# Optimization experiments

Measured on AMD Instinct MI355X. Metric: run time of the kernel, lower is better.

The kernel has to match this reference:

```python
import jax, jax.numpy as jnp
import numpy as np

N = 50000


def gcn_conv(x, W, b, src, dst, deg_inv_sqrt):
    # h = x @ W, then symmetric-normalized aggregation with self-loops
    h = x @ W  # [N, out]
    norm = deg_inv_sqrt[src] * deg_inv_sqrt[dst]  # [E]
    agg = jax.ops.segment_sum(h[src] * norm[:, None], dst, num_segments=N)
    # self-loop contribution: norm_ii = deg_inv_sqrt[i]^2
    agg = agg + h * (deg_inv_sqrt * deg_inv_sqrt)[:, None]
    return agg + b


def setup_inputs() -> dict:
    key = jax.random.key(0)
    ks = jax.random.split(key, 8)
    F_in, H, C = 128, 128, 64
    x = jax.random.normal(ks[0], (N, F_in), dtype=jnp.float32)
    edge_index = jax.random.randint(ks[1], (2, 800000), 0, N, dtype=jnp.int64)
    s = 1.0 / np.sqrt(F_in)
    W1 = jax.random.uniform(ks[2], (F_in, H), jnp.float32, -s, s)
    b1 = jnp.zeros((H,), jnp.float32)
    W2 = jax.random.uniform(ks[3], (H, H), jnp.float32, -s, s)
    b2 = jnp.zeros((H,), jnp.float32)
    W3 = jax.random.uniform(ks[4], (H, C), jnp.float32, -s, s)
    b3 = jnp.zeros((C,), jnp.float32)
    return {"x": x, "edge_index": edge_index, "W1": W1, "b1": b1,
            "W2": W2, "b2": b2, "W3": W3, "b3": b3}


def reference(x, edge_index, W1, b1, W2, b2, W3, b3):
    src, dst = edge_index[0], edge_index[1]
    # degree with self-loops (edge weight 1): deg[i] = in-degree + 1
    deg = jnp.zeros((N,), x.dtype).at[dst].add(1.0) + 1.0
    dinv = jax.lax.rsqrt(deg)
    h = gcn_conv(x, W1, b1, src, dst, dinv)
    h = jax.nn.relu(h)  # dropout p=0 / eval -> identity
    h = gcn_conv(h, W2, b2, src, dst, dinv)
    h = jax.nn.relu(h)
    h = gcn_conv(h, W3, b3, src, dst, dinv)
    return jax.nn.log_softmax(h, axis=-1)
```

## Files before the change

kernel.cpp:

```cpp
#include <hip/hip_runtime.h>
#include <math.h>

typedef short short8 __attribute__((ext_vector_type(8)));
typedef float floatx4 __attribute__((ext_vector_type(4)));

__device__ __forceinline__ float4 ld4(const float* p) { return *reinterpret_cast<const float4*>(p); }
__device__ __forceinline__ void st4(float* p, float4 v) { *reinterpret_cast<float4*>(p) = v; }

__device__ __forceinline__ float bf2f(unsigned int u) { return __uint_as_float(u << 16); }
__device__ __forceinline__ unsigned int f2bf1(float f) {
    unsigned int x = __float_as_uint(f);
    return (x + 0x7fffu + ((x >> 16) & 1u)) >> 16;
}
__device__ __forceinline__ unsigned int f2bf2(float lo, float hi) {
    return f2bf1(lo) | (f2bf1(hi) << 16);
}
__device__ __forceinline__ void unpack8(uint4 v, float* f) {
    f[0] = bf2f(v.x & 0xffffu); f[1] = bf2f(v.x >> 16);
    f[2] = bf2f(v.y & 0xffffu); f[3] = bf2f(v.y >> 16);
    f[4] = bf2f(v.z & 0xffffu); f[5] = bf2f(v.z >> 16);
    f[6] = bf2f(v.w & 0xffffu); f[7] = bf2f(v.w >> 16);
}

__global__ __launch_bounds__(256) void k_count_prep(const int* __restrict__ dst, int* __restrict__ deg,
                                                    int* __restrict__ rank, int E, int nbE,
                                                    const float* __restrict__ W1, const float* __restrict__ W2,
                                                    const float* __restrict__ W3, unsigned short* __restrict__ Wt1,
                                                    unsigned short* __restrict__ Wt2, unsigned short* __restrict__ Wt3) {
    if ((int)blockIdx.x < nbE) {
        int e = blockIdx.x * 256 + threadIdx.x;
        if (e < E) rank[e] = atomicAdd(&deg[dst[e]], 1);
    } else {
        int t = (blockIdx.x - nbE) * 256 + threadIdx.x;
        if (t < 16384) {
            int k = t & 127, n = t >> 7;
            Wt1[n * 128 + k] = (unsigned short)f2bf1(W1[(size_t)k * 128 + n]);
        } else if (t < 32768) {
            int u = t - 16384;
            int k = u & 127, n = u >> 7;
            Wt2[n * 128 + k] = (unsigned short)f2bf1(W2[(size_t)k * 128 + n]);
        } else if (t < 40960) {
            int u = t - 32768;
            int k = u & 127, n = u >> 7;
            Wt3[n * 128 + k] = (unsigned short)f2bf1(W3[(size_t)k * 64 + n]);
        }
    }
}

__global__ __launch_bounds__(256) void k_dinv_reduce(const int* __restrict__ deg, float* __restrict__ dinv,
                                                     int* __restrict__ bsum, int n, int nbN) {
    __shared__ int s[256];
    int t = threadIdx.x;
    if ((int)blockIdx.x < nbN) {
        int i = blockIdx.x * 256 + t;
        if (i < n) dinv[i] = 1.0f / sqrtf((float)deg[i] + 1.0f);
        return;
    }
    int b = (int)blockIdx.x - nbN;
    int i = b * 256 + t;
    s[t] = (i < n) ? deg[i] : 0;
    __syncthreads();
    for (int off = 128; off > 0; off >>= 1) {
        if (t < off) s[t] += s[t + off];
        __syncthreads();
    }
    if (t == 0) bsum[b] = s[0];
}

__global__ __launch_bounds__(256) void k_scansmall_gemm1(const int* __restrict__ bsum, int* __restrict__ boff, int nb,
                                                         const float* __restrict__ X, const unsigned short* __restrict__ Wt,
                                                         const float* __restrict__ dinv,
                                                         unsigned short* __restrict__ O, int nrows) {
    constexpr int LDR = 136;
    __shared__ __align__(16) unsigned char smem[(64 * LDR + 128 * LDR) * 2];

    const int tid = threadIdx.x;
    if (blockIdx.x == 0) {
        int* s = (int*)smem;
        int v = (tid < nb) ? bsum[tid] : 0;
        s[tid] = v;
        __syncthreads();
        for (int off = 1; off < 256; off <<= 1) {
            int x = (tid >= off) ? s[tid - off] : 0;
            __syncthreads();
            s[tid] += x;
            __syncthreads();
        }
        if (tid < nb) boff[tid] = s[tid] - v;
        return;
    }

    unsigned short* sX = (unsigned short*)smem;
    unsigned short* sB = sX + 64 * LDR;
    const int row0 = ((int)blockIdx.x - 1) * 64;

#pragma unroll
    for (int i = 0; i < 4; ++i) {
        int idx = tid + i * 256;
        int r = idx >> 4, c8 = idx & 15;
        int grow = row0 + r;
        uint4 v = make_uint4(0, 0, 0, 0);
        if (grow < nrows) {
            float4 a = ld4(X + (size_t)grow * 128 + c8 * 8);
            float4 b = ld4(X + (size_t)grow * 128 + c8 * 8 + 4);
            v = make_uint4(f2bf2(a.x, a.y), f2bf2(a.z, a.w), f2bf2(b.x, b.y), f2bf2(b.z, b.w));
        }
        *reinterpret_cast<uint4*>(&sX[r * LDR + c8 * 8]) = v;
    }
#pragma unroll
    for (int i = 0; i < 8; ++i) {
        int idx = tid + i * 256;
        int nn = idx >> 4, c8 = idx & 15;
        *reinterpret_cast<uint4*>(&sB[nn * LDR + c8 * 8]) =
            *reinterpret_cast<const uint4*>(Wt + (size_t)nn * 128 + c8 * 8);
    }
    __syncthreads();

    const int lane = tid & 63;
    const int wave = tid >> 6;
    const int l15  = lane & 15;
    const int quad = lane >> 4;

    floatx4 acc[8];
#pragma unroll
    for (int j = 0; j < 8; ++j) acc[j] = (floatx4){0.f, 0.f, 0.f, 0.f};

    const unsigned short* xbase = &sX[(wave * 16 + l15) * LDR + quad * 8];
#pragma unroll
    for (int kk = 0; kk < 4; ++kk) {
        short8 xb = *reinterpret_cast<const short8*>(xbase + kk * 32);
#pragma unroll
        for (int j = 0; j < 8; ++j) {
            short8 wa = *reinterpret_cast<const short8*>(&sB[(j * 16 + l15) * LDR + quad * 8 + kk * 32]);
            acc[j] = __builtin_amdgcn_mfma_f32_16x16x32_bf16(wa, xb, acc[j], 0, 0, 0);
        }
    }

    int xrow = row0 + wave * 16 + l15;
    if (xrow < nrows) {
        float di = dinv[xrow];
#pragma unroll
        for (int j = 0; j < 8; ++j) {
            uint2 o = make_uint2(f2bf2(acc[j][0] * di, acc[j][1] * di), f2bf2(acc[j][2] * di, acc[j][3] * di));
            *reinterpret_cast<uint2*>(O + (size_t)xrow * 128 + j * 16 + quad * 4) = o;
        }
    }
}

__global__ __launch_bounds__(256) void k_scan_final(const int* __restrict__ deg, const int* __restrict__ boff,
                                                    int* __restrict__ row_off, int n) {
    __shared__ int s[256];
    int t = threadIdx.x;
    int i = blockIdx.x * 256 + t;
    int v = (i < n) ? deg[i] : 0;
    s[t] = v;
    __syncthreads();
    for (int off = 1; off < 256; off <<= 1) {
        int x = (t >= off) ? s[t - off] : 0;
        __syncthreads();
        s[t] += x;
        __syncthreads();
    }
    int incl = s[t] + boff[blockIdx.x];
    if (i < n) {
        row_off[i] = incl - v;
        if (i == n - 1) row_off[n] = incl;
    }
}

__global__ __launch_bounds__(256) void k_fill(const int* __restrict__ src, const int* __restrict__ dst,
                                              const int* __restrict__ rank, const int* __restrict__ roff,
                                              int* __restrict__ csrc, int E) {
    int e = blockIdx.x * 256 + threadIdx.x;
    if (e < E) csrc[roff[dst[e]] + rank[e]] = src[e];
}

template <int NC>
__global__ __launch_bounds__(256) void k_gemm_mfma(const unsigned short* __restrict__ X,
                                                   const unsigned short* __restrict__ Wt,
                                                   const float* __restrict__ dinv,
                                                   unsigned short* __restrict__ O, int nrows) {
    constexpr int LDR = 136;
    __shared__ unsigned short sX[64 * LDR];
    __shared__ unsigned short sB[NC * LDR];

    const int tid  = threadIdx.x;
    const int row0 = blockIdx.x * 64;

#pragma unroll
    for (int i = 0; i < 4; ++i) {
        int idx = tid + i * 256;
        int r = idx >> 4, c8 = idx & 15;
        int grow = row0 + r;
        uint4 v = make_uint4(0, 0, 0, 0);
        if (grow < nrows) v = *reinterpret_cast<const uint4*>(X + (size_t)grow * 128 + c8 * 8);
        *reinterpret_cast<uint4*>(&sX[r * LDR + c8 * 8]) = v;
    }
#pragma unroll
    for (int i = 0; i < NC / 16; ++i) {
        int idx = tid + i * 256;
        int n = idx >> 4, c8 = idx & 15;
        *reinterpret_cast<uint4*>(&sB[n * LDR + c8 * 8]) =
            *reinterpret_cast<const uint4*>(Wt + (size_t)n * 128 + c8 * 8);
    }
    __syncthreads();

    const int lane = tid & 63;
    const int wave = tid >> 6;
    const int l15  = lane & 15;
    const int quad = lane >> 4;

    floatx4 acc[NC / 16];
#pragma unroll
    for (int j = 0; j < NC / 16; ++j) acc[j] = (floatx4){0.f, 0.f, 0.f, 0.f};

    const unsigned short* xbase = &sX[(wave * 16 + l15) * LDR + quad * 8];
#pragma unroll
    for (int kk = 0; kk < 4; ++kk) {
        short8 xb = *reinterpret_cast<const short8*>(xbase + kk * 32);
#pragma unroll
        for (int j = 0; j < NC / 16; ++j) {
            short8 wa = *reinterpret_cast<const short8*>(&sB[(j * 16 + l15) * LDR + quad * 8 + kk * 32]);
            acc[j] = __builtin_amdgcn_mfma_f32_16x16x32_bf16(wa, xb, acc[j], 0, 0, 0);
        }
    }

    int xrow = row0 + wave * 16 + l15;
    if (xrow < nrows) {
        float di = dinv[xrow];
#pragma unroll
        for (int j = 0; j < NC / 16; ++j) {
            uint2 o = make_uint2(f2bf2(acc[j][0] * di, acc[j][1] * di), f2bf2(acc[j][2] * di, acc[j][3] * di));
            *reinterpret_cast<uint2*>(O + (size_t)xrow * NC + j * 16 + quad * 4) = o;
        }
    }
}

__global__ __launch_bounds__(256) void k_agg_relu(const unsigned short* __restrict__ H, const int* __restrict__ roff,
                                                  const int* __restrict__ csrc, const float* __restrict__ dinv,
                                                  const float* __restrict__ bias, unsigned short* __restrict__ O, int n) {
    int t      = blockIdx.x * 256 + threadIdx.x;
    int node   = t >> 5;
    int lane32 = t & 31;
    int half   = lane32 >> 4;
    int f8     = (lane32 & 15) * 8;
    if (node >= n) return;

    float a[8];
    if (half == 0) {
        uint4 hv = *reinterpret_cast<const uint4*>(H + (size_t)node * 128 + f8);
        unpack8(hv, a);
    } else {
#pragma unroll
        for (int i = 0; i < 8; ++i) a[i] = 0.0f;
    }

    int e0 = roff[node];
    int e1 = roff[node + 1];
    int mid = e0 + ((e1 - e0) >> 1);
    int e  = half ? mid : e0;
    int ee = half ? e1 : mid;

    while (e < ee) {
        int cnt = ee - e;
        int idx[8];
#pragma unroll
        for (int u = 0; u < 8; ++u) idx[u] = csrc[e + min(u, cnt - 1)];
        uint4 v[8];
#pragma unroll
        for (int u = 0; u < 8; ++u) v[u] = *reinterpret_cast<const uint4*>(H + (size_t)idx[u] * 128 + f8);
#pragma unroll
        for (int u = 0; u < 8; ++u) {
            float mk = (u < cnt) ? 1.0f : 0.0f;
            float g[8];
            unpack8(v[u], g);
#pragma unroll
            for (int i = 0; i < 8; ++i) a[i] = fmaf(mk, g[i], a[i]);
        }
        e += 8;
    }

#pragma unroll
    for (int i = 0; i < 8; ++i) a[i] += __shfl_xor(a[i], 16);

    if (half == 0) {
        float di = dinv[node];
        float4 b0 = ld4(bias + f8);
        float4 b1 = ld4(bias + f8 + 4);
        float bb[8] = {b0.x, b0.y, b0.z, b0.w, b1.x, b1.y, b1.z, b1.w};
#pragma unroll
        for (int i = 0; i < 8; ++i) a[i] = fmaxf(a[i] * di + bb[i], 0.0f);

        uint4 ov = make_uint4(f2bf2(a[0], a[1]), f2bf2(a[2], a[3]), f2bf2(a[4], a[5]), f2bf2(a[6], a[7]));
        *reinterpret_cast<uint4*>(O + (size_t)node * 128 + f8) = ov;
    }
}

__global__ __launch_bounds__(256) void k_agg_softmax(const unsigned short* __restrict__ H, const int* __restrict__ roff,
                                                     const int* __restrict__ csrc, const float* __restrict__ dinv,
                                                     const float* __restrict__ bias, float* __restrict__ O, int n) {
    int t      = blockIdx.x * 256 + threadIdx.x;
    int node   = t >> 4;
    int lane16 = t & 15;
    int half   = lane16 >> 3;
    int f8     = (lane16 & 7) * 8;
    if (node >= n) return;

    float a[8];
    if (half == 0) {
        uint4 hv = *reinterpret_cast<const uint4*>(H + (size_t)node * 64 + f8);
        unpack8(hv, a);
    } else {
#pragma unroll
        for (int i = 0; i < 8; ++i) a[i] = 0.0f;
    }

    int e0 = roff[node];
    int e1 = roff[node + 1];
    int mid = e0 + ((e1 - e0) >> 1);
    int e  = half ? mid : e0;
    int ee = half ? e1 : mid;

    while (e < ee) {
        int cnt = ee - e;
        int idx[8];
#pragma unroll
        for (int u = 0; u < 8; ++u) idx[u] = csrc[e + min(u, cnt - 1)];
        uint4 v[8];
#pragma unroll
        for (int u = 0; u < 8; ++u) v[u] = *reinterpret_cast<const uint4*>(H + (size_t)idx[u] * 64 + f8);
#pragma unroll
        for (int u = 0; u < 8; ++u) {
            float mk = (u < cnt) ? 1.0f : 0.0f;
            float g[8];
            unpack8(v[u], g);
#pragma unroll
            for (int i = 0; i < 8; ++i) a[i] = fmaf(mk, g[i], a[i]);
        }
        e += 8;
    }

#pragma unroll
    for (int i = 0; i < 8; ++i) a[i] += __shfl_xor(a[i], 8);

    if (half == 0) {
        float di = dinv[node];
        float4 b0 = ld4(bias + f8);
        float4 b1 = ld4(bias + f8 + 4);
        float bb[8] = {b0.x, b0.y, b0.z, b0.w, b1.x, b1.y, b1.z, b1.w};
        float v[8];
#pragma unroll
        for (int i = 0; i < 8; ++i) v[i] = a[i] * di + bb[i];

        float m = v[0];
#pragma unroll
        for (int i = 1; i < 8; ++i) m = fmaxf(m, v[i]);
        m = fmaxf(m, __shfl_xor(m, 1));
        m = fmaxf(m, __shfl_xor(m, 2));
        m = fmaxf(m, __shfl_xor(m, 4));

        float ssum = 0.0f;
#pragma unroll
        for (int i = 0; i < 8; ++i) ssum += expf(v[i] - m);
        ssum += __shfl_xor(ssum, 1);
        ssum += __shfl_xor(ssum, 2);
        ssum += __shfl_xor(ssum, 4);
        float ls = logf(ssum);

        float* op = O + (size_t)node * 64 + f8;
        st4(op, make_float4(v[0] - m - ls, v[1] - m - ls, v[2] - m - ls, v[3] - m - ls));
        st4(op + 4, make_float4(v[4] - m - ls, v[5] - m - ls, v[6] - m - ls, v[7] - m - ls));
    }
}

extern "C" void kernel_launch(void* const* d_in, const int* in_sizes, int n_in,
                              void* d_out, int out_size, void* d_ws, size_t ws_size,
                              hipStream_t stream) {
    const float* x  = (const float*)d_in[0];
    const int*   ei = (const int*)d_in[1];
    const float* W1 = (const float*)d_in[2];
    const float* b1 = (const float*)d_in[3];
    const float* W2 = (const float*)d_in[4];
    const float* b2 = (const float*)d_in[5];
    const float* W3 = (const float*)d_in[6];
    const float* b3 = (const float*)d_in[7];
    float* out = (float*)d_out;

    const int N = in_sizes[0] / 128;
    const int E = in_sizes[1] / 2;
    const int* src = ei;
    const int* dst = ei + E;

    char* ws = (char*)d_ws;
    size_t off = 0;
    auto alloc = [&](size_t bytes) -> char* {
        char* p = ws + off;
        off = (off + bytes + 255) & ~(size_t)255;
        return p;
    };
    int nb  = (N + 255) / 256;
    int nbE = (E + 255) / 256;
    int blocks64 = (N + 63) / 64;

    int*   deg     = (int*)alloc((size_t)N * 4);
    int*   row_off = (int*)alloc(((size_t)N + 1) * 4);
    float* dinv    = (float*)alloc((size_t)N * 4);
    int*   bsum    = (int*)alloc((size_t)nb * 4);
    int*   boff    = (int*)alloc((size_t)nb * 4);
    int*   rank    = (int*)alloc((size_t)E * 4);
    int*   csrc    = (int*)alloc((size_t)E * 4);
    unsigned short* Wt1  = (unsigned short*)alloc(128 * 128 * 2);
    unsigned short* Wt2  = (unsigned short*)alloc(128 * 128 * 2);
    unsigned short* Wt3  = (unsigned short*)alloc(64 * 128 * 2);
    unsigned short* bufA = (unsigned short*)alloc((size_t)N * 128 * 2);
    unsigned short* bufB = (unsigned short*)alloc((size_t)N * 128 * 2);
    unsigned short* bufC = (unsigned short*)alloc((size_t)N * 64 * 2);
    (void)ws_size; (void)n_in; (void)out_size;

    hipMemsetAsync(deg, 0, (size_t)N * 4, stream);
    k_count_prep<<<nbE + 160, 256, 0, stream>>>(dst, deg, rank, E, nbE, W1, W2, W3, Wt1, Wt2, Wt3);
    k_dinv_reduce<<<nb + nb, 256, 0, stream>>>(deg, dinv, bsum, N, nb);
    k_scansmall_gemm1<<<1 + blocks64, 256, 0, stream>>>(bsum, boff, nb, x, Wt1, dinv, bufA, N);
    k_scan_final<<<nb, 256, 0, stream>>>(deg, boff, row_off, N);
    k_fill<<<nbE, 256, 0, stream>>>(src, dst, rank, row_off, csrc, E);

    k_agg_relu<<<((size_t)N * 32 + 255) / 256, 256, 0, stream>>>(bufA, row_off, csrc, dinv, b1, bufB, N);
    k_gemm_mfma<128><<<blocks64, 256, 0, stream>>>(bufB, Wt2, dinv, bufA, N);
    k_agg_relu<<<((size_t)N * 32 + 255) / 256, 256, 0, stream>>>(bufA, row_off, csrc, dinv, b2, bufB, N);
    k_gemm_mfma<64><<<blocks64, 256, 0, stream>>>(bufB, Wt3, dinv, bufC, N);
    k_agg_softmax<<<((size_t)N * 16 + 255) / 256, 256, 0, stream>>>(bufC, row_off, csrc, dinv, b3, out, N);
}
```

Baseline: 257.5 us.

## Replace multi-kernel scan with single-pass decoupled lookback scan and fuse fill with GEMM1

Replaces the reduce, small-scan and final-scan kernels with a single-pass decoupled-lookback scan that also writes dinv. The CSR fill is merged into the first GEMM launch as extra blocks. The aggregation loops now unroll by 4 with a scalar tail instead of 8-wide masked gathers. The aim is fewer launches and serial stages in preprocessing and less wasted gather work on short edge lists. The lookback spin-wait depends on earlier blocks being scheduled first, which is not guaranteed.

```diff
diff --git a/kernel.cpp b/kernel.cpp
--- a/kernel.cpp
+++ b/kernel.cpp
@@ -47,52 +47,62 @@
     }
 }
 
-__global__ __launch_bounds__(256) void k_dinv_reduce(const int* __restrict__ deg, float* __restrict__ dinv,
-                                                     int* __restrict__ bsum, int n, int nbN) {
+__global__ __launch_bounds__(256) void k_scan_dinv(const int* __restrict__ deg, int* __restrict__ state,
+                                                   int* __restrict__ row_off, float* __restrict__ dinv, int n) {
     __shared__ int s[256];
-    int t = threadIdx.x;
-    if ((int)blockIdx.x < nbN) {
-        int i = blockIdx.x * 256 + t;
-        if (i < n) dinv[i] = 1.0f / sqrtf((float)deg[i] + 1.0f);
-        return;
-    }
-    int b = (int)blockIdx.x - nbN;
-    int i = b * 256 + t;
-    s[t] = (i < n) ? deg[i] : 0;
+    __shared__ int sbase;
+    const int bid = (int)blockIdx.x;
+    const int t = threadIdx.x;
+    int i = bid * 256 + t;
+    int v = (i < n) ? deg[i] : 0;
+    s[t] = v;
     __syncthreads();
-    for (int off = 128; off > 0; off >>= 1) {
-        if (t < off) s[t] += s[t + off];
+    for (int off = 1; off < 256; off <<= 1) {
+        int x = (t >= off) ? s[t - off] : 0;
         __syncthreads();
-    }
-    if (t == 0) bsum[b] = s[0];
-}
-
-__global__ __launch_bounds__(256) void k_scansmall_gemm1(const int* __restrict__ bsum, int* __restrict__ boff, int nb,
-                                                         const float* __restrict__ X, const unsigned short* __restrict__ Wt,
-                                                         const float* __restrict__ dinv,
-                                                         unsigned short* __restrict__ O, int nrows) {
+        s[t] += x;
+        __syncthreads();
+    }
+    const int bsum = s[255];
+    if (t == 0) {
+        atomicExch(&state[bid], (int)((1u << 30) | (unsigned)bsum));
+        int run = 0;
+        for (int j = bid - 1; j >= 0; --j) {
+            int st;
+            do { st = atomicAdd(&state[j], 0); } while ((unsigned)st < (1u << 30));
+            run += st & 0x3fffffff;
+            if (((unsigned)st >> 30) == 2u) break;
+        }
+        atomicExch(&state[bid], (int)((2u << 30) | (unsigned)(run + bsum)));
+        sbase = run;
+    }
+    __syncthreads();
+    if (i < n) {
+        row_off[i] = sbase + s[t] - v;
+        dinv[i] = 1.0f / sqrtf((float)v + 1.0f);
+        if (i == n - 1) row_off[n] = sbase + bsum;
+    }
+}
+
+__global__ __launch_bounds__(256) void k_fill_gemm1(const int* __restrict__ src, const int* __restrict__ dst,
+                                                    const int* __restrict__ rank, const int* __restrict__ roff,
+                                                    int* __restrict__ csrc, int E, int nbE,
+                                                    const float* __restrict__ X, const unsigned short* __restrict__ Wt,
+                                                    const float* __restrict__ dinv,
+                                                    unsigned short* __restrict__ O, int nrows) {
     constexpr int LDR = 136;
     __shared__ __align__(16) unsigned char smem[(64 * LDR + 128 * LDR) * 2];
-
     const int tid = threadIdx.x;
-    if (blockIdx.x == 0) {
-        int* s = (int*)smem;
-        int v = (tid < nb) ? bsum[tid] : 0;
-        s[tid] = v;
-        __syncthreads();
-        for (int off = 1; off < 256; off <<= 1) {
-            int x = (tid >= off) ? s[tid - off] : 0;
-            __syncthreads();
-            s[tid] += x;
-            __syncthreads();
-        }
-        if (tid < nb) boff[tid] = s[tid] - v;
+
+    if ((int)blockIdx.x < nbE) {
+        int e = blockIdx.x * 256 + tid;
+        if (e < E) csrc[roff[dst[e]] + rank[e]] = src[e];
         return;
     }
 
     unsigned short* sX = (unsigned short*)smem;
     unsigned short* sB = sX + 64 * LDR;
-    const int row0 = ((int)blockIdx.x - 1) * 64;
+    const int row0 = ((int)blockIdx.x - nbE) * 64;
 
 #pragma unroll
     for (int i = 0; i < 4; ++i) {
@@ -147,34 +157,6 @@
     }
 }
 
-__global__ __launch_bounds__(256) void k_scan_final(const int* __restrict__ deg, const int* __restrict__ boff,
-                                                    int* __restrict__ row_off, int n) {
-    __shared__ int s[256];
-    int t = threadIdx.x;
-    int i = blockIdx.x * 256 + t;
-    int v = (i < n) ? deg[i] : 0;
-    s[t] = v;
-    __syncthreads();
-    for (int off = 1; off < 256; off <<= 1) {
-        int x = (t >= off) ? s[t - off] : 0;
-        __syncthreads();
-        s[t] += x;
-        __syncthreads();
-    }
-    int incl = s[t] + boff[blockIdx.x];
-    if (i < n) {
-        row_off[i] = incl - v;
-        if (i == n - 1) row_off[n] = incl;
-    }
-}
-
-__global__ __launch_bounds__(256) void k_fill(const int* __restrict__ src, const int* __restrict__ dst,
-                                              const int* __restrict__ rank, const int* __restrict__ roff,
-                                              int* __restrict__ csrc, int E) {
-    int e = blockIdx.x * 256 + threadIdx.x;
-    if (e < E) csrc[roff[dst[e]] + rank[e]] = src[e];
-}
-
 template <int NC>
 __global__ __launch_bounds__(256) void k_gemm_mfma(const unsigned short* __restrict__ X,
                                                    const unsigned short* __restrict__ Wt,
@@ -261,23 +243,27 @@
     int e  = half ? mid : e0;
     int ee = half ? e1 : mid;
 
-    while (e < ee) {
-        int cnt = ee - e;
-        int idx[8];
-#pragma unroll
-        for (int u = 0; u < 8; ++u) idx[u] = csrc[e + min(u, cnt - 1)];
-        uint4 v[8];
-#pragma unroll
-        for (int u = 0; u < 8; ++u) v[u] = *reinterpret_cast<const uint4*>(H + (size_t)idx[u] * 128 + f8);
-#pragma unroll
-        for (int u = 0; u < 8; ++u) {
-            float mk = (u < cnt) ? 1.0f : 0.0f;
-            float g[8];
-            unpack8(v[u], g);
-#pragma unroll
-            for (int i = 0; i < 8; ++i) a[i] = fmaf(mk, g[i], a[i]);
-        }
-        e += 8;
+    for (; e + 3 < ee; e += 4) {
+        int s[4];
+        uint4 v[4];
+#pragma unroll
+        for (int u = 0; u < 4; ++u) s[u] = csrc[e + u];
+#pragma unroll
+        for (int u = 0; u < 4; ++u) v[u] = *reinterpret_cast<const uint4*>(H + (size_t)s[u] * 128 + f8);
+#pragma unroll
+        for (int u = 0; u < 4; ++u) {
+            float g2[8];
+            unpack8(v[u], g2);
+#pragma unroll
+            for (int i = 0; i < 8; ++i) a[i] += g2[i];
+        }
+    }
+    for (; e < ee; ++e) {
+        uint4 v0 = *reinterpret_cast<const uint4*>(H + (size_t)csrc[e] * 128 + f8);
+        float g0[8];
+        unpack8(v0, g0);
+#pragma unroll
+        for (int i = 0; i < 8; ++i) a[i] += g0[i];
     }
 
 #pragma unroll
@@ -321,23 +307,27 @@
     int e  = half ? mid : e0;
     int ee = half ? e1 : mid;
 
-    while (e < ee) {
-        int cnt = ee - e;
-        int idx[8];
-#pragma unroll
-        for (int u = 0; u < 8; ++u) idx[u] = csrc[e + min(u, cnt - 1)];
-        uint4 v[8];
-#pragma unroll
-        for (int u = 0; u < 8; ++u) v[u] = *reinterpret_cast<const uint4*>(H + (size_t)idx[u] * 64 + f8);
-#pragma unroll
-        for (int u = 0; u < 8; ++u) {
-            float mk = (u < cnt) ? 1.0f : 0.0f;
-            float g[8];
-            unpack8(v[u], g);
-#pragma unroll
-            for (int i = 0; i < 8; ++i) a[i] = fmaf(mk, g[i], a[i]);
-        }
-        e += 8;
+    for (; e + 3 < ee; e += 4) {
+        int s[4];
+        uint4 v[4];
+#pragma unroll
+        for (int u = 0; u < 4; ++u) s[u] = csrc[e + u];
+#pragma unroll
+        for (int u = 0; u < 4; ++u) v[u] = *reinterpret_cast<const uint4*>(H + (size_t)s[u] * 64 + f8);
+#pragma unroll
+        for (int u = 0; u < 4; ++u) {
+            float gg[8];
+            unpack8(v[u], gg);
+#pragma unroll
+            for (int i = 0; i < 8; ++i) a[i] += gg[i];
+        }
+    }
+    for (; e < ee; ++e) {
+        uint4 v0 = *reinterpret_cast<const uint4*>(H + (size_t)csrc[e] * 64 + f8);
+        float g0[8];
+        unpack8(v0, g0);
+#pragma unroll
+        for (int i = 0; i < 8; ++i) a[i] += g0[i];
     }
 
 #pragma unroll
@@ -403,10 +393,9 @@
     int blocks64 = (N + 63) / 64;
 
     int*   deg     = (int*)alloc((size_t)N * 4);
+    int*   state   = (int*)alloc((size_t)nb * 4);
     int*   row_off = (int*)alloc(((size_t)N + 1) * 4);
     float* dinv    = (float*)alloc((size_t)N * 4);
-    int*   bsum    = (int*)alloc((size_t)nb * 4);
-    int*   boff    = (int*)alloc((size_t)nb * 4);
     int*   rank    = (int*)alloc((size_t)E * 4);
     int*   csrc    = (int*)alloc((size_t)E * 4);
     unsigned short* Wt1  = (unsigned short*)alloc(128 * 128 * 2);
@@ -417,12 +406,14 @@
     unsigned short* bufC = (unsigned short*)alloc((size_t)N * 64 * 2);
     (void)ws_size; (void)n_in; (void)out_size;
 
-    hipMemsetAsync(deg, 0, (size_t)N * 4, stream);
+    size_t degPad   = (((size_t)N * 4 + 255) & ~(size_t)255);
+    size_t statePad = (((size_t)nb * 4 + 255) & ~(size_t)255);
+    hipMemsetAsync(deg, 0, degPad + statePad, stream);
+
     k_count_prep<<<nbE + 160, 256, 0, stream>>>(dst, deg, rank, E, nbE, W1, W2, W3, Wt1, Wt2, Wt3);
-    k_dinv_reduce<<<nb + nb, 256, 0, stream>>>(deg, dinv, bsum, N, nb);
-    k_scansmall_gemm1<<<1 + blocks64, 256, 0, stream>>>(bsum, boff, nb, x, Wt1, dinv, bufA, N);
-    k_scan_final<<<nb, 256, 0, stream>>>(deg, boff, row_off, N);
-    k_fill<<<nbE, 256, 0, stream>>>(src, dst, rank, row_off, csrc, E);
+    k_scan_dinv<<<nb, 256, 0, stream>>>(deg, state, row_off, dinv, N);
+    k_fill_gemm1<<<nbE + blocks64, 256, 0, stream>>>(src, dst, rank, row_off, csrc, E, nbE,
+                                                     x, Wt1, dinv, bufA, N);
 
     k_agg_relu<<<((size_t)N * 32 + 255) / 256, 256, 0, stream>>>(bufA, row_off, csrc, dinv, b1, bufB, N);
     k_gemm_mfma<128><<<blocks64, 256, 0, stream>>>(bufB, Wt2, dinv, bufA, N);
```

Measured after the change: 261.4 us. Within noise of the previous version (+1.5%).
